# Kernel tuning notes

Hardware: AMD Instinct MI355X
Metric: run time of the kernel (lower is better)

The kernel has to match this reference:

```python
import jax, jax.numpy as jnp
import numpy as np
from jax import lax

N, CIN, H, W = 16, 3, 512, 512
BH = BW = 16  # block size (h, w); bstride == bsize so blocks tile the image
EPS = 1e-5


def setup_inputs() -> dict:
    key = jax.random.key(0)
    ks = jax.random.split(key, 32)
    def nrm(k, shape, s=0.05):
        return jax.random.normal(k, shape, jnp.float32) * s
    def bnp(k, ch):
        # rows: gamma, beta, running_mean, running_var (var kept > 0)
        u = jax.random.uniform(k, (4, ch), jnp.float32)
        return u.at[3].add(0.1)
    feat = (H // 4) * (W // 4) * 8
    return {
        "x": jax.random.normal(ks[0], (N, CIN, H, W), jnp.float32),
        "mask": jax.random.uniform(ks[1], (N, 1, H, W), jnp.float32),
        "s1_cw": nrm(ks[2], (16, CIN, 1, 1)), "s1_cb": nrm(ks[3], (16,)), "s1_bn0": bnp(ks[4], 16),
        "s1_d1w": nrm(ks[5], (32, 16, 1, 1)), "s1_d1b": nrm(ks[6], (32,)), "s1_bn1": bnp(ks[7], 32),
        "s1_d2w": nrm(ks[8], (32, 32, 3, 3)), "s1_d2b": nrm(ks[9], (32,)), "s1_bn2": bnp(ks[10], 32),
        "s1_d3w": nrm(ks[11], (16, 32, 1, 1)), "s1_d3b": nrm(ks[12], (16,)), "s1_bn3": bnp(ks[13], 16),
        "s2_cw": nrm(ks[14], (8, 16, 1, 1)), "s2_cb": nrm(ks[15], (8,)), "s2_bn0": bnp(ks[16], 8),
        "s2_d1w": nrm(ks[17], (16, 8, 1, 1)), "s2_d1b": nrm(ks[18], (16,)), "s2_bn1": bnp(ks[19], 16),
        "s2_d2w": nrm(ks[20], (16, 16, 3, 3)), "s2_d2b": nrm(ks[21], (16,)), "s2_bn2": bnp(ks[22], 16),
        "s2_d3w": nrm(ks[23], (8, 16, 1, 1)), "s2_d3b": nrm(ks[24], (8,)), "s2_bn3": bnp(ks[25], 8),
        "fc_w": nrm(ks[26], (10, feat), 0.01), "fc_b": nrm(ks[27], (10,)),
    }


def conv(x, w, b, p):
    y = lax.conv_general_dilated(x, w, (1, 1), [(p, p), (p, p)],
                                 dimension_numbers=("NCHW", "OIHW", "NCHW"))
    return y + b[None, :, None, None]


def bnorm(x, p):
    g, bt, m, v = p[0], p[1], p[2], p[3]
    scale = g * lax.rsqrt(v + EPS)
    return scale[None, :, None, None] * (x - m[None, :, None, None]) + bt[None, :, None, None]


def to_blocks(x):
    # [N,C,H,W] -> [N*nby*nbx, C, BH, BW]
    n, c, hh, ww = x.shape
    nby, nbx = hh // BH, ww // BW
    b = x.reshape(n, c, nby, BH, nbx, BW).transpose(0, 2, 4, 1, 3, 5)
    return b.reshape(n * nby * nbx, c, BH, BW), (n, nby, nbx)


def from_blocks(b, meta, c):
    n, nby, nbx = meta
    x = b.reshape(n, nby, nbx, c, BH, BW).transpose(0, 3, 1, 4, 2, 5)
    return x.reshape(n, c, nby * BH, nbx * BW)


def maxpool2(x):
    return lax.reduce_window(x, -jnp.inf, lax.max, (1, 1, 2, 2), (1, 1, 2, 2), "VALID")


def sparse_conv_block(x, mask, cw, cb, bn0, d1w, d1b, bn1, d2w, d2b, bn2, d3w, d3b, bn3):
    # reduce_mask: block is active if its mean mask value exceeds threshold
    mblocks, _ = to_blocks(mask)
    active = mblocks.mean(axis=(1, 2, 3)) > 0.5  # [N*nblocks]
    # channel path (applies to every pixel)
    xc = bnorm(jax.nn.relu(conv(x, cw, cb, 0)), bn0)
    # gather -> dense bottleneck convs per block (3x3 padded within each block) -> scatter
    blocks, meta = to_blocks(xc)
    g = bnorm(jax.nn.relu(conv(blocks, d1w, d1b, 0)), bn1)
    g = bnorm(jax.nn.relu(conv(g, d2w, d2b, 1)), bn2)
    g = bnorm(jax.nn.relu(conv(g, d3w, d3b, 0)), bn3)
    out = jnp.where(active[:, None, None, None], g, blocks)
    return from_blocks(out, meta, xc.shape[1])


def reference(x, mask, s1_cw, s1_cb, s1_bn0, s1_d1w, s1_d1b, s1_bn1, s1_d2w, s1_d2b, s1_bn2,
              s1_d3w, s1_d3b, s1_bn3, s2_cw, s2_cb, s2_bn0, s2_d1w, s2_d1b, s2_bn1,
              s2_d2w, s2_d2b, s2_bn2, s2_d3w, s2_d3b, s2_bn3, fc_w, fc_b):
    x1 = sparse_conv_block(x, mask, s1_cw, s1_cb, s1_bn0, s1_d1w, s1_d1b, s1_bn1,
                           s1_d2w, s1_d2b, s1_bn2, s1_d3w, s1_d3b, s1_bn3)
    x1 = maxpool2(x1)
    mask2 = maxpool2(mask)
    x2 = sparse_conv_block(x1, mask2, s2_cw, s2_cb, s2_bn0, s2_d1w, s2_d1b, s2_bn1,
                           s2_d2w, s2_d2b, s2_bn2, s2_d3w, s2_d3b, s2_bn3)
    x2 = maxpool2(x2)
    flat = x2.reshape(x2.shape[0], -1)  # [N, (H/4)*(W/4)*8]
    logits = flat @ fc_w.T + fc_b
    return jax.nn.softmax(logits, axis=-1)
```

## Files before the change

### kernel.cpp

```cpp
#include <hip/hip_runtime.h>
#include <math.h>


typedef __attribute__((ext_vector_type(8))) short bf16x8;
typedef __attribute__((ext_vector_type(4))) float f32x4;
typedef __attribute__((ext_vector_type(16))) float f32x16;

#define X1P_OFF 0
#define X2_OFF  16777216
#define LG_OFF  18874368
#define MS_OFF  18874624
#define P_OFF   18878720

enum : int {
  WT_S1C  = 0,
  WT_S2C  = 48,
  SC_S1BN0 = 176,
  SC_S1BN1 = 208,
  SC_S1BN2 = 272,
  SC_S1BN3 = 336,
  SC_S2BN0 = 368,
  SC_S2BN1 = 384,
  SC_S2BN2 = 416,
  SC_S2BN3 = 448,
  PH_F     = 464
};
enum : int {
  H_S1D2 = 0,
  H_S1D3 = 9216,
  H_S2D2 = 9728,
  H_S2D3 = 12288,
  H_S1D1 = 12544,
  H_S2D1 = 13568,
  PH_END = 14080
};

__device__ __forceinline__ float relu_f(float v) { return v > 0.f ? v : 0.f; }

__device__ __forceinline__ unsigned short f2bf(float f) {
  unsigned int u = __float_as_uint(f);
  unsigned int r = (u + 0x7fffu + ((u >> 16) & 1u)) >> 16;
  return (unsigned short)r;
}

__device__ __forceinline__ unsigned int pk2(float lo, float hi) {
  unsigned int r;
  asm("v_cvt_pk_bf16_f32 %0, %1, %2" : "=v"(r) : "v"(lo), "v"(hi));
  return r;
}

__device__ __forceinline__ void prep_bn(const float* __restrict__ p, int C,
                                        float* __restrict__ dst, int gid) {
  for (int i = gid; i < C; i += 8192) {
    float g = p[i], b = p[C + i], m = p[2 * C + i], v = p[3 * C + i];
    float s = g / sqrtf(v + 1e-5f);
    dst[i] = s;
    dst[C + i] = b - s * m;
  }
}

__global__ __launch_bounds__(256) void prep_kernel(
    const float* __restrict__ s1_cw, const float* __restrict__ s1_d1w,
    const float* __restrict__ s1_d2w, const float* __restrict__ s1_d3w,
    const float* __restrict__ s2_cw, const float* __restrict__ s2_d1w,
    const float* __restrict__ s2_d2w, const float* __restrict__ s2_d3w,
    const float* __restrict__ s1_bn0, const float* __restrict__ s1_bn1,
    const float* __restrict__ s1_bn2, const float* __restrict__ s1_bn3,
    const float* __restrict__ s2_bn0, const float* __restrict__ s2_bn1,
    const float* __restrict__ s2_bn2, const float* __restrict__ s2_bn3,
    float* __restrict__ P, float* __restrict__ lg, float* __restrict__ ms) {
  const int gid = blockIdx.x * 256 + threadIdx.x;
  unsigned short* PH = (unsigned short*)(P + PH_F);
  for (int i = gid; i < 48;  i += 8192) { int co = i / 3,  ci = i % 3;  P[WT_S1C + ci * 16 + co] = s1_cw[i]; }
  for (int i = gid; i < 128; i += 8192) { int co = i / 16, ci = i % 16; P[WT_S2C + ci * 8  + co] = s2_cw[i]; }
  for (int i = gid; i < 9216; i += 8192) {
    int tap = i >> 10, o = (i >> 5) & 31, ci = i & 31;
    PH[H_S1D2 + i] = f2bf(s1_d2w[o * 288 + ci * 9 + tap]);
  }
  for (int i = gid; i < 512; i += 8192) PH[H_S1D3 + i] = f2bf(s1_d3w[i]);
  for (int i = gid; i < 2560; i += 8192) {
    int p = i >> 9, o = (i >> 5) & 15, k = i & 31;
    int tp = 2 * p + (k >> 4);
    PH[H_S2D2 + i] = (tp < 9) ? f2bf(s2_d2w[o * 144 + (k & 15) * 9 + tp]) : 0;
  }
  for (int i = gid; i < 256; i += 8192) {
    int nn = i >> 4, k = i & 15;
    PH[H_S2D3 + i] = (nn < 8) ? f2bf(s2_d3w[nn * 16 + k]) : 0;
  }
  for (int i = gid; i < 1024; i += 8192) {
    int o = i >> 5, k = i & 31;
    PH[H_S1D1 + i] = (k < 16) ? f2bf(s1_d1w[o * 16 + k]) : 0;
  }
  for (int i = gid; i < 512; i += 8192) {
    int o = i >> 5, k = i & 31;
    PH[H_S2D1 + i] = (k < 8) ? f2bf(s2_d1w[o * 8 + k]) : 0;
  }
  prep_bn(s1_bn0, 16, P + SC_S1BN0, gid);
  prep_bn(s1_bn1, 32, P + SC_S1BN1, gid);
  prep_bn(s1_bn2, 32, P + SC_S1BN2, gid);
  prep_bn(s1_bn3, 16, P + SC_S1BN3, gid);
  prep_bn(s2_bn0, 8,  P + SC_S2BN0, gid);
  prep_bn(s2_bn1, 16, P + SC_S2BN1, gid);
  prep_bn(s2_bn2, 16, P + SC_S2BN2, gid);
  prep_bn(s2_bn3, 8,  P + SC_S2BN3, gid);
  if (gid < 160) lg[gid] = 0.f;
  for (int i = gid; i < 4096; i += 8192) ms[i] = 0.f;
}

__global__ __launch_bounds__(256, 4) void stage1_kernel(
    const float* __restrict__ x, const float* __restrict__ mask,
    const float* __restrict__ cbv, const float* __restrict__ d1b,
    const float* __restrict__ d2b, const float* __restrict__ d3b,
    const float* __restrict__ P, float* __restrict__ x1p,
    float* __restrict__ msum) {
  __shared__ __align__(16) unsigned char ldsb[25920];
  __shared__ float red_s[4], red_v[4];

  const int t = threadIdx.x;
  const int ty = t >> 4, tx = t & 15;
  const int b = blockIdx.x;
  const int n = b >> 10;
  const int by = (b >> 5) & 31, bx = b & 31;
  const int gy = by * 16 + ty, gx = bx * 16 + tx;

  {
    const float m = mask[(size_t)(n * 512 + gy) * 512 + gx];
    float v = fmaxf(m, __shfl_xor(m, 1, 64));
    v = fmaxf(v, __shfl_xor(v, 16, 64));
    float s = m;
    #pragma unroll
    for (int off = 32; off > 0; off >>= 1) {
      s += __shfl_down(s, off, 64);
      v += __shfl_down(v, off, 64);
    }
    if ((t & 63) == 0) { red_s[t >> 6] = s; red_v[t >> 6] = v; }
  }
  __syncthreads();

  float xin[3];
  #pragma unroll
  for (int c = 0; c < 3; ++c)
    xin[c] = x[(size_t)((n * 3 + c) * 512 + gy) * 512 + gx];

  const float* wc = P + WT_S1C;
  const float* sc0 = P + SC_S1BN0;
  float xc[16];
  {
    float a[16];
    #pragma unroll
    for (int o = 0; o < 16; ++o) a[o] = cbv[o];
    #pragma unroll
    for (int c = 0; c < 3; ++c) {
      const float v = xin[c];
      #pragma unroll
      for (int o = 0; o < 16; ++o) a[o] = fmaf(wc[c * 16 + o], v, a[o]);
    }
    #pragma unroll
    for (int o = 0; o < 16; ++o) xc[o] = fmaf(sc0[o], relu_f(a[o]), sc0[16 + o]);
  }

  const bool active = (red_s[0] + red_s[1] + red_s[2] + red_s[3]) > 128.0f;
  if (t == 0)
    atomicAdd(&msum[n * 256 + (by >> 1) * 16 + (bx >> 1)],
              (red_v[0] + red_v[1] + red_v[2] + red_v[3]) * 0.25f);

  float* const poolf = (float*)(ldsb + 20480);

  if (active) {
    const int w = t >> 6, lane = t & 63;
    const int lr = lane & 15, cb = lane >> 4;
    const unsigned short* PH = (const unsigned short*)(P + PH_F);

    if (t < 68) {
      int row, col;
      if (t < 18)      { row = 0;      col = t;      }
      else if (t < 36) { row = 17;     col = t - 18; }
      else if (t < 52) { row = t - 35; col = 0;      }
      else             { row = t - 51; col = 17;     }
      uint4* z = (uint4*)(ldsb + (row * 18 + col) * 80);
      const uint4 z4 = make_uint4(0u, 0u, 0u, 0u);
      z[0] = z4; z[1] = z4; z[2] = z4; z[3] = z4;
    }
    {
      unsigned int pk[8];
      #pragma unroll
      for (int i = 0; i < 8; ++i) pk[i] = pk2(xc[2 * i], xc[2 * i + 1]);
      uint4* dst = (uint4*)(ldsb + ((ty + 1) * 18 + (tx + 1)) * 80);
      dst[0] = make_uint4(pk[0], pk[1], pk[2], pk[3]);
      dst[1] = make_uint4(pk[4], pk[5], pk[6], pk[7]);
    }

    {
      bf16x8 w1f[2];
      #pragma unroll
      for (int ct = 0; ct < 2; ++ct)
        w1f[ct] = *(const bf16x8*)(PH + H_S1D1 + (ct * 16 + lr) * 32 + cb * 8);
      f32x4 acc1[2][4];
      #pragma unroll
      for (int ct = 0; ct < 2; ++ct) {
        const float4 bb = *(const float4*)(d1b + ct * 16 + cb * 4);
        #pragma unroll
        for (int nt = 0; nt < 4; ++nt) {
          acc1[ct][nt][0] = bb.x; acc1[ct][nt][1] = bb.y;
          acc1[ct][nt][2] = bb.z; acc1[ct][nt][3] = bb.w;
        }
      }
      #pragma unroll
      for (int nt = 0; nt < 4; ++nt) {
        bf16x8 xcf;
        if (cb < 2) xcf = *(const bf16x8*)(ldsb + ((w * 4 + nt + 1) * 18 + lr + 1) * 80 + cb * 16);
        else        xcf = (bf16x8)(short)0;
        #pragma unroll
        for (int ct = 0; ct < 2; ++ct)
          acc1[ct][nt] = __builtin_amdgcn_mfma_f32_16x16x32_bf16(w1f[ct], xcf, acc1[ct][nt], 0, 0, 0);
      }
      #pragma unroll
      for (int ct = 0; ct < 2; ++ct) {
        const float4 s1s = *(const float4*)(P + SC_S1BN1 + ct * 16 + cb * 4);
        const float4 s1h = *(const float4*)(P + SC_S1BN1 + 32 + ct * 16 + cb * 4);
        #pragma unroll
        for (int nt = 0; nt < 4; ++nt) {
          const unsigned base = ((w * 4 + nt + 1) * 18 + lr + 1) * 80 + (ct * 16 + cb * 4) * 2;
          uint2 wv;
          wv.x = pk2(fmaf(s1s.x, relu_f(acc1[ct][nt][0]), s1h.x),
                     fmaf(s1s.y, relu_f(acc1[ct][nt][1]), s1h.y));
          wv.y = pk2(fmaf(s1s.z, relu_f(acc1[ct][nt][2]), s1h.z),
                     fmaf(s1s.w, relu_f(acc1[ct][nt][3]), s1h.w));
          *(uint2*)(ldsb + base) = wv;
        }
      }
    }
    __syncthreads();

    const int lane31 = lane & 31;
    const int prow = lane31 >> 4, pcol = lane & 15, kh = lane >> 5;
    f32x16 acc2[2];
    {
      float4 bb2[4];
      #pragma unroll
      for (int g = 0; g < 4; ++g) bb2[g] = *(const float4*)(d2b + 8 * g + 4 * kh);
      #pragma unroll
      for (int mti = 0; mti < 2; ++mti) {
        #pragma unroll
        for (int g = 0; g < 4; ++g) {
          acc2[mti][4 * g + 0] = bb2[g].x; acc2[mti][4 * g + 1] = bb2[g].y;
          acc2[mti][4 * g + 2] = bb2[g].z; acc2[mti][4 * g + 3] = bb2[g].w;
        }
      }
    }
    #pragma clang loop unroll(disable)
    for (int dy = 0; dy < 3; ++dy) {
      bf16x8 aw[3][2];
      #pragma unroll
      for (int dx = 0; dx < 3; ++dx)
        #pragma unroll
        for (int ch = 0; ch < 2; ++ch)
          aw[dx][ch] = *(const bf16x8*)(PH + H_S1D2 + ((dy * 3 + dx) * 32 + lane31) * 32 + ch * 16 + kh * 8);
      const unsigned char* bp = ldsb + ((w * 4 + prow + dy) * 18 + pcol) * 80 + kh * 16;
      #pragma unroll
      for (int dx = 0; dx < 3; ++dx)
        #pragma unroll
        for (int mti = 0; mti < 2; ++mti)
          #pragma unroll
          for (int ch = 0; ch < 2; ++ch) {
            const bf16x8 bf = *(const bf16x8*)(bp + mti * 2880 + dx * 80 + ch * 32);
            acc2[mti] = __builtin_amdgcn_mfma_f32_32x32x16_bf16(aw[dx][ch], bf, acc2[mti], 0, 0, 0);
          }
    }
    __syncthreads();

    #pragma unroll
    for (int mti = 0; mti < 2; ++mti) {
      const int pix = (w * 2 + mti) * 32 + lane31;
      #pragma unroll
      for (int g = 0; g < 4; ++g) {
        const float4 ss = *(const float4*)(P + SC_S1BN2 + 8 * g + 4 * kh);
        const float4 sh = *(const float4*)(P + SC_S1BN2 + 32 + 8 * g + 4 * kh);
        uint2 wv;
        wv.x = pk2(fmaf(ss.x, relu_f(acc2[mti][4 * g + 0]), sh.x),
                   fmaf(ss.y, relu_f(acc2[mti][4 * g + 1]), sh.y));
        wv.y = pk2(fmaf(ss.z, relu_f(acc2[mti][4 * g + 2]), sh.z),
                   fmaf(ss.w, relu_f(acc2[mti][4 * g + 3]), sh.w));
        *(uint2*)(ldsb + pix * 80 + (8 * g + 4 * kh) * 2) = wv;
      }
    }
    __syncthreads();

    const bf16x8 b3 = *(const bf16x8*)(PH + H_S1D3 + lr * 32 + cb * 8);
    const float bias3v = d3b[lr];
    const float sc3v = P[SC_S1BN3 + lr], sh3v = P[SC_S1BN3 + 16 + lr];
    f32x4 acc3[4];
    #pragma unroll
    for (int mt = 0; mt < 4; ++mt) {
      acc3[mt][0] = bias3v; acc3[mt][1] = bias3v; acc3[mt][2] = bias3v; acc3[mt][3] = bias3v;
      const bf16x8 a3 = *(const bf16x8*)(ldsb + (w * 64 + mt * 16 + lr) * 80 + cb * 16);
      acc3[mt] = __builtin_amdgcn_mfma_f32_16x16x32_bf16(a3, b3, acc3[mt], 0, 0, 0);
    }
    #pragma unroll
    for (int mtp = 0; mtp < 2; ++mtp) {
      float o0[4], o1[4];
      #pragma unroll
      for (int r = 0; r < 4; ++r) {
        o0[r] = fmaf(sc3v, relu_f(acc3[2 * mtp][r]), sh3v);
        o1[r] = fmaf(sc3v, relu_f(acc3[2 * mtp + 1][r]), sh3v);
      }
      #pragma unroll
      for (int rp = 0; rp < 2; ++rp) {
        const float m = fmaxf(fmaxf(o0[2 * rp], o0[2 * rp + 1]),
                              fmaxf(o1[2 * rp], o1[2 * rp + 1]));
        poolf[lr * 68 + (w * 2 + mtp) * 8 + cb * 2 + rp] = m;
      }
    }
  } else {
    float* ldsf = (float*)ldsb;
    {
      float* pw = &ldsf[t * 20];
      #pragma unroll
      for (int c = 0; c < 16; ++c) pw[c] = xc[c];
    }
    __syncthreads();
    {
      const int pp = t & 63, cg = t >> 6;
      const int py = pp >> 3, px = pp & 7;
      const float* r0 = &ldsf[((2 * py) * 16 + 2 * px) * 20 + cg * 4];
      const float* r2 = &ldsf[((2 * py + 1) * 16 + 2 * px) * 20 + cg * 4];
      const float4 v0 = *(const float4*)(r0);
      const float4 v1 = *(const float4*)(r0 + 20);
      const float4 v2 = *(const float4*)(r2);
      const float4 v3 = *(const float4*)(r2 + 20);
      poolf[(cg * 4 + 0) * 68 + py * 8 + px] = fmaxf(fmaxf(v0.x, v1.x), fmaxf(v2.x, v3.x));
      poolf[(cg * 4 + 1) * 68 + py * 8 + px] = fmaxf(fmaxf(v0.y, v1.y), fmaxf(v2.y, v3.y));
      poolf[(cg * 4 + 2) * 68 + py * 8 + px] = fmaxf(fmaxf(v0.z, v1.z), fmaxf(v2.z, v3.z));
      poolf[(cg * 4 + 3) * 68 + py * 8 + px] = fmaxf(fmaxf(v0.w, v1.w), fmaxf(v2.w, v3.w));
    }
  }

  __syncthreads();
  {
    const int ch = t >> 4, idx = t & 15, yy = idx >> 1, h = idx & 1;
    const uint4 v = *(const uint4*)(poolf + ch * 68 + yy * 8 + h * 4);
    const size_t ob = ((((size_t)n * 16 + (by >> 1)) * 16 + (bx >> 1)) * 16 + ch) * 256
                      + (size_t)((by & 1) * 8 + yy) * 16 + (bx & 1) * 8 + h * 4;
    *(uint4*)(x1p + ob) = v;
  }
}

__global__ __launch_bounds__(256, 5) void stage2_kernel(
    const float* __restrict__ msum,
    const float* __restrict__ cbv, const float* __restrict__ d1b,
    const float* __restrict__ d2b, const float* __restrict__ d3b,
    const float* __restrict__ P, const float* __restrict__ x1p,
    float* __restrict__ x2) {
  __shared__ __align__(16) unsigned char ldsb2[15552];

  const int t = threadIdx.x;
  const int ty = t >> 4, tx = t & 15;
  const int b = blockIdx.x;
  const int n = b >> 8;
  const int BY = (b >> 4) & 15, BX = b & 15;

  const bool active = msum[b] > 128.0f;

  const float* xb = x1p + (size_t)b * 4096 + ty * 16 + tx;
  float xin[16];
  #pragma unroll
  for (int c = 0; c < 16; ++c) xin[c] = xb[c * 256];

  const float* wc = P + WT_S2C;
  const float* sc0 = P + SC_S2BN0;
  float xc[8];
  {
    float a[8];
    #pragma unroll
    for (int o = 0; o < 8; ++o) a[o] = cbv[o];
    #pragma unroll
    for (int c = 0; c < 16; ++c) {
      const float v = xin[c];
      #pragma unroll
      for (int o = 0; o < 8; ++o) a[o] = fmaf(wc[c * 8 + o], v, a[o]);
    }
    #pragma unroll
    for (int o = 0; o < 8; ++o) xc[o] = fmaf(sc0[o], relu_f(a[o]), sc0[8 + o]);
  }

  float* const poolf = (float*)(ldsb2 + 12288);

  if (active) {
    const int w = t >> 6, lane = t & 63;
    const int lr = lane & 15, cb = lane >> 4;
    const unsigned short* PH = (const unsigned short*)(P + PH_F);

    if (t < 68) {
      int row, col;
      if (t < 18)      { row = 0;      col = t;      }
      else if (t < 36) { row = 17;     col = t - 18; }
      else if (t < 52) { row = t - 35; col = 0;      }
      else             { row = t - 51; col = 17;     }
      uint4* z = (uint4*)(ldsb2 + (row * 18 + col) * 48);
      const uint4 z4 = make_uint4(0u, 0u, 0u, 0u);
      z[0] = z4; z[1] = z4;
    }
    {
      unsigned int pk[4];
      #pragma unroll
      for (int i = 0; i < 4; ++i) pk[i] = pk2(xc[2 * i], xc[2 * i + 1]);
      *(uint4*)(ldsb2 + ((ty + 1) * 18 + (tx + 1)) * 48) = make_uint4(pk[0], pk[1], pk[2], pk[3]);
    }

    {
      const bf16x8 w1f = *(const bf16x8*)(PH + H_S2D1 + lr * 32 + cb * 8);
      f32x4 acc1[4];
      {
        const float4 bb = *(const float4*)(d1b + cb * 4);
        #pragma unroll
        for (int nt = 0; nt < 4; ++nt) {
          acc1[nt][0] = bb.x; acc1[nt][1] = bb.y; acc1[nt][2] = bb.z; acc1[nt][3] = bb.w;
        }
      }
      #pragma unroll
      for (int nt = 0; nt < 4; ++nt) {
        bf16x8 xcf;
        if (cb == 0) xcf = *(const bf16x8*)(ldsb2 + ((w * 4 + nt + 1) * 18 + lr + 1) * 48);
        else         xcf = (bf16x8)(short)0;
        acc1[nt] = __builtin_amdgcn_mfma_f32_16x16x32_bf16(w1f, xcf, acc1[nt], 0, 0, 0);
      }
      {
        const float4 s1s = *(const float4*)(P + SC_S2BN1 + cb * 4);
        const float4 s1h = *(const float4*)(P + SC_S2BN1 + 16 + cb * 4);
        #pragma unroll
        for (int nt = 0; nt < 4; ++nt) {
          const unsigned base = ((w * 4 + nt + 1) * 18 + lr + 1) * 48 + cb * 8;
          uint2 wv;
          wv.x = pk2(fmaf(s1s.x, relu_f(acc1[nt][0]), s1h.x),
                     fmaf(s1s.y, relu_f(acc1[nt][1]), s1h.y));
          wv.y = pk2(fmaf(s1s.z, relu_f(acc1[nt][2]), s1h.z),
                     fmaf(s1s.w, relu_f(acc1[nt][3]), s1h.w));
          *(uint2*)(ldsb2 + base) = wv;
        }
      }
    }
    __syncthreads();

    f32x4 acc2[4];
    {
      const float4 bb = *(const float4*)(d2b + cb * 4);
      #pragma unroll
      for (int nt = 0; nt < 4; ++nt) {
        acc2[nt][0] = bb.x; acc2[nt][1] = bb.y; acc2[nt][2] = bb.z; acc2[nt][3] = bb.w;
      }
    }
    #pragma clang loop unroll(disable)
    for (int p = 0; p < 5; ++p) {
      const bf16x8 bwp = *(const bf16x8*)(PH + H_S2D2 + (p * 16 + lr) * 32 + cb * 8);
      const int tp = (p < 4) ? (2 * p + (cb >> 1)) : 8;
      const int dy = (tp >= 6) ? 2 : ((tp >= 3) ? 1 : 0);
      const int dx = tp - dy * 3;
      #pragma unroll
      for (int nt = 0; nt < 4; ++nt) {
        const bf16x8 af = *(const bf16x8*)(ldsb2 + ((w * 4 + nt + dy) * 18 + lr + dx) * 48 + (cb & 1) * 16);
        acc2[nt] = __builtin_amdgcn_mfma_f32_16x16x32_bf16(bwp, af, acc2[nt], 0, 0, 0);
      }
    }
    __syncthreads();

    {
      const float4 s2s = *(const float4*)(P + SC_S2BN2 + cb * 4);
      const float4 s2h = *(const float4*)(P + SC_S2BN2 + 16 + cb * 4);
      #pragma unroll
      for (int nt = 0; nt < 4; ++nt) {
        const int pix = w * 64 + nt * 16 + lr;
        const unsigned base = pix * 48 + cb * 8;
        uint2 wv;
        wv.x = pk2(fmaf(s2s.x, relu_f(acc2[nt][0]), s2h.x),
                   fmaf(s2s.y, relu_f(acc2[nt][1]), s2h.y));
        wv.y = pk2(fmaf(s2s.z, relu_f(acc2[nt][2]), s2h.z),
                   fmaf(s2s.w, relu_f(acc2[nt][3]), s2h.w));
        *(uint2*)(ldsb2 + base) = wv;
      }
    }
    __syncthreads();

    bf16x8 b3;
    if (cb < 2) b3 = *(const bf16x8*)(PH + H_S2D3 + lr * 16 + cb * 8);
    else        b3 = (bf16x8)(short)0;
    const float bias3v = (lr < 8) ? d3b[lr] : 0.f;
    const float sc3v = (lr < 8) ? P[SC_S2BN3 + lr] : 0.f;
    const float sh3v = (lr < 8) ? P[SC_S2BN3 + 8 + lr] : 0.f;
    f32x4 acc3[4];
    #pragma unroll
    for (int mt = 0; mt < 4; ++mt) {
      acc3[mt][0] = bias3v; acc3[mt][1] = bias3v; acc3[mt][2] = bias3v; acc3[mt][3] = bias3v;
      bf16x8 a3;
      if (cb < 2) a3 = *(const bf16x8*)(ldsb2 + (w * 64 + mt * 16 + lr) * 48 + cb * 16);
      else        a3 = (bf16x8)(short)0;
      acc3[mt] = __builtin_amdgcn_mfma_f32_16x16x32_bf16(a3, b3, acc3[mt], 0, 0, 0);
    }
    if (lr < 8) {
      #pragma unroll
      for (int mtp = 0; mtp < 2; ++mtp) {
        float o0[4], o1[4];
        #pragma unroll
        for (int r = 0; r < 4; ++r) {
          o0[r] = fmaf(sc3v, relu_f(acc3[2 * mtp][r]), sh3v);
          o1[r] = fmaf(sc3v, relu_f(acc3[2 * mtp + 1][r]), sh3v);
        }
        #pragma unroll
        for (int rp = 0; rp < 2; ++rp) {
          const float m = fmaxf(fmaxf(o0[2 * rp], o0[2 * rp + 1]),
                                fmaxf(o1[2 * rp], o1[2 * rp + 1]));
          poolf[lr * 68 + (w * 2 + mtp) * 8 + cb * 2 + rp] = m;
        }
      }
    }
  } else {
    float* ldsf = (float*)ldsb2;
    {
      float* pw = &ldsf[t * 12];
      #pragma unroll
      for (int c = 0; c < 8; ++c) pw[c] = xc[c];
    }
    __syncthreads();
    if (t < 128) {
      const int pp = t & 63, cg = t >> 6;
      const int py = pp >> 3, px = pp & 7;
      const float* r0 = &ldsf[((2 * py) * 16 + 2 * px) * 12 + cg * 4];
      const float* r2 = &ldsf[((2 * py + 1) * 16 + 2 * px) * 12 + cg * 4];
      const float4 v0 = *(const float4*)(r0);
      const float4 v1 = *(const float4*)(r0 + 12);
      const float4 v2 = *(const float4*)(r2);
      const float4 v3 = *(const float4*)(r2 + 12);
      poolf[(cg * 4 + 0) * 68 + py * 8 + px] = fmaxf(fmaxf(v0.x, v1.x), fmaxf(v2.x, v3.x));
      poolf[(cg * 4 + 1) * 68 + py * 8 + px] = fmaxf(fmaxf(v0.y, v1.y), fmaxf(v2.y, v3.y));
      poolf[(cg * 4 + 2) * 68 + py * 8 + px] = fmaxf(fmaxf(v0.z, v1.z), fmaxf(v2.z, v3.z));
      poolf[(cg * 4 + 3) * 68 + py * 8 + px] = fmaxf(fmaxf(v0.w, v1.w), fmaxf(v2.w, v3.w));
    }
  }

  __syncthreads();
  if (t < 128) {
    const int ch = t >> 4, idx = t & 15, yy = idx >> 1, h = idx & 1;
    const uint4 v = *(const uint4*)(poolf + ch * 68 + yy * 8 + h * 4);
    const size_t ob = ((size_t)(n * 8 + ch) * 128 + (BY * 8 + yy)) * 128 + BX * 8 + h * 4;
    *(uint4*)(x2 + ob) = v;
  }
}

__global__ __launch_bounds__(256) void fc_kernel(const float* __restrict__ x2,
                                                 const float* __restrict__ fcw,
                                                 const float* __restrict__ fcb,
                                                 float* __restrict__ logits) {
  __shared__ float red[4];
  const int wg = blockIdx.x, t = threadIdx.x;
  const int sp = wg & 7, k = (wg >> 3) % 10, n = wg / 80;
  const float4* xa = (const float4*)(x2 + (size_t)n * 131072) + sp * 4096;
  const float4* wa = (const float4*)(fcw + (size_t)k * 131072) + sp * 4096;
  float s = 0.f;
  #pragma unroll 4
  for (int i = t; i < 4096; i += 256) {
    const float4 a = xa[i], b = wa[i];
    s = fmaf(a.x, b.x, fmaf(a.y, b.y, fmaf(a.z, b.z, fmaf(a.w, b.w, s))));
  }
  #pragma unroll
  for (int off = 32; off > 0; off >>= 1) s += __shfl_down(s, off, 64);
  if ((t & 63) == 0) red[t >> 6] = s;
  __syncthreads();
  if (t == 0) {
    float tot = red[0] + red[1] + red[2] + red[3];
    if (sp == 0) tot += fcb[k];
    atomicAdd(&logits[n * 10 + k], tot);
  }
}

__global__ void softmax_kernel(const float* __restrict__ logits, float* __restrict__ out) {
  const int t = threadIdx.x;
  if (t < 16) {
    float l[10], mx = -1e30f;
    #pragma unroll
    for (int k = 0; k < 10; ++k) { l[k] = logits[t * 10 + k]; mx = fmaxf(mx, l[k]); }
    float sum = 0.f;
    #pragma unroll
    for (int k = 0; k < 10; ++k) { l[k] = expf(l[k] - mx); sum += l[k]; }
    const float inv = 1.f / sum;
    #pragma unroll
    for (int k = 0; k < 10; ++k) out[t * 10 + k] = l[k] * inv;
  }
}

extern "C" void kernel_launch(void* const* d_in, const int* in_sizes, int n_in,
                              void* d_out, int out_size, void* d_ws, size_t ws_size,
                              hipStream_t stream) {
  const float* x      = (const float*)d_in[0];
  const float* mask   = (const float*)d_in[1];
  const float* s1_cw  = (const float*)d_in[2];
  const float* s1_cb  = (const float*)d_in[3];
  const float* s1_bn0 = (const float*)d_in[4];
  const float* s1_d1w = (const float*)d_in[5];
  const float* s1_d1b = (const float*)d_in[6];
  const float* s1_bn1 = (const float*)d_in[7];
  const float* s1_d2w = (const float*)d_in[8];
  const float* s1_d2b = (const float*)d_in[9];
  const float* s1_bn2 = (const float*)d_in[10];
  const float* s1_d3w = (const float*)d_in[11];
  const float* s1_d3b = (const float*)d_in[12];
  const float* s1_bn3 = (const float*)d_in[13];
  const float* s2_cw  = (const float*)d_in[14];
  const float* s2_cb  = (const float*)d_in[15];
  const float* s2_bn0 = (const float*)d_in[16];
  const float* s2_d1w = (const float*)d_in[17];
  const float* s2_d1b = (const float*)d_in[18];
  const float* s2_bn1 = (const float*)d_in[19];
  const float* s2_d2w = (const float*)d_in[20];
  const float* s2_d2b = (const float*)d_in[21];
  const float* s2_bn2 = (const float*)d_in[22];
  const float* s2_d3w = (const float*)d_in[23];
  const float* s2_d3b = (const float*)d_in[24];
  const float* s2_bn3 = (const float*)d_in[25];
  const float* fc_w   = (const float*)d_in[26];
  const float* fc_b   = (const float*)d_in[27];

  float* ws  = (float*)d_ws;
  float* x1p = ws + X1P_OFF;
  float* x2  = ws + X2_OFF;
  float* lg  = ws + LG_OFF;
  float* ms  = ws + MS_OFF;
  float* P   = ws + P_OFF;

  prep_kernel<<<32, 256, 0, stream>>>(s1_cw, s1_d1w, s1_d2w, s1_d3w,
                                      s2_cw, s2_d1w, s2_d2w, s2_d3w,
                                      s1_bn0, s1_bn1, s1_bn2, s1_bn3,
                                      s2_bn0, s2_bn1, s2_bn2, s2_bn3, P, lg, ms);
  stage1_kernel<<<16 * 32 * 32, 256, 0, stream>>>(x, mask, s1_cb, s1_d1b, s1_d2b, s1_d3b, P, x1p, ms);
  stage2_kernel<<<16 * 16 * 16, 256, 0, stream>>>(ms, s2_cb, s2_d1b, s2_d2b, s2_d3b, P, x1p, x2);
  fc_kernel<<<1280, 256, 0, stream>>>(x2, fc_w, fc_b, lg);
  softmax_kernel<<<1, 64, 0, stream>>>(lg, (float*)d_out);
}
```

Baseline: 276.4 us.

## Store pooled stage-1 output as bf16 and use 32x32 MFMA for 1x1 convs

The pooled intermediate between stage 1 and stage 2 is now written and read as bf16 instead of fp32, which halves that tensor's global memory traffic and shrinks the workspace. The first 1x1 bottleneck conv in both stages switches from 16x16x32 MFMA tiles with zero-padded K to 32x32x16 MFMA tiles, with the weight packing in the prep kernel changed to match. This cuts wasted MFMA work on padding, but adds bf16 rounding on an activation that was previously kept in fp32.

```diff
diff --git a/kernel.cpp b/kernel.cpp
--- a/kernel.cpp
+++ b/kernel.cpp
@@ -6,11 +6,11 @@
 typedef __attribute__((ext_vector_type(4))) float f32x4;
 typedef __attribute__((ext_vector_type(16))) float f32x16;
 
-#define X1P_OFF 0
-#define X2_OFF  16777216
-#define LG_OFF  18874368
-#define MS_OFF  18874624
-#define P_OFF   18878720
+#define X1P_USH_OFF 0
+#define X2_OFF  8388608
+#define LG_OFF  10485760
+#define MS_OFF  10486016
+#define P_OFF   10490112
 
 enum : int {
   WT_S1C  = 0,
@@ -49,6 +49,10 @@
   return r;
 }
 
+__device__ __forceinline__ float bf2f(unsigned short u) {
+  return __uint_as_float((unsigned int)u << 16);
+}
+
 __device__ __forceinline__ void prep_bn(const float* __restrict__ p, int C,
                                         float* __restrict__ dst, int gid) {
   for (int i = gid; i < C; i += 8192) {
@@ -87,13 +91,10 @@
     int nn = i >> 4, k = i & 15;
     PH[H_S2D3 + i] = (nn < 8) ? f2bf(s2_d3w[nn * 16 + k]) : 0;
   }
-  for (int i = gid; i < 1024; i += 8192) {
-    int o = i >> 5, k = i & 31;
-    PH[H_S1D1 + i] = (k < 16) ? f2bf(s1_d1w[o * 16 + k]) : 0;
-  }
+  for (int i = gid; i < 512; i += 8192) PH[H_S1D1 + i] = f2bf(s1_d1w[i]);
   for (int i = gid; i < 512; i += 8192) {
-    int o = i >> 5, k = i & 31;
-    PH[H_S2D1 + i] = (k < 8) ? f2bf(s2_d1w[o * 8 + k]) : 0;
+    int co = i >> 4, k = i & 15;
+    PH[H_S2D1 + i] = (co < 16 && k < 8) ? f2bf(s2_d1w[co * 8 + k]) : 0;
   }
   prep_bn(s1_bn0, 16, P + SC_S1BN0, gid);
   prep_bn(s1_bn1, 32, P + SC_S1BN1, gid);
@@ -111,7 +112,7 @@
     const float* __restrict__ x, const float* __restrict__ mask,
     const float* __restrict__ cbv, const float* __restrict__ d1b,
     const float* __restrict__ d2b, const float* __restrict__ d3b,
-    const float* __restrict__ P, float* __restrict__ x1p,
+    const float* __restrict__ P, unsigned short* __restrict__ x1p,
     float* __restrict__ msum) {
   __shared__ __align__(16) unsigned char ldsb[25920];
   __shared__ float red_s[4], red_v[4];
@@ -169,6 +170,7 @@
   if (active) {
     const int w = t >> 6, lane = t & 63;
     const int lr = lane & 15, cb = lane >> 4;
+    const int lane31 = lane & 31, kh = lane >> 5;
     const unsigned short* PH = (const unsigned short*)(P + PH_F);
 
     if (t < 68) {
@@ -191,49 +193,42 @@
     }
 
     {
-      bf16x8 w1f[2];
-      #pragma unroll
-      for (int ct = 0; ct < 2; ++ct)
-        w1f[ct] = *(const bf16x8*)(PH + H_S1D1 + (ct * 16 + lr) * 32 + cb * 8);
-      f32x4 acc1[2][4];
-      #pragma unroll
-      for (int ct = 0; ct < 2; ++ct) {
-        const float4 bb = *(const float4*)(d1b + ct * 16 + cb * 4);
-        #pragma unroll
-        for (int nt = 0; nt < 4; ++nt) {
-          acc1[ct][nt][0] = bb.x; acc1[ct][nt][1] = bb.y;
-          acc1[ct][nt][2] = bb.z; acc1[ct][nt][3] = bb.w;
-        }
-      }
-      #pragma unroll
-      for (int nt = 0; nt < 4; ++nt) {
-        bf16x8 xcf;
-        if (cb < 2) xcf = *(const bf16x8*)(ldsb + ((w * 4 + nt + 1) * 18 + lr + 1) * 80 + cb * 16);
-        else        xcf = (bf16x8)(short)0;
-        #pragma unroll
-        for (int ct = 0; ct < 2; ++ct)
-          acc1[ct][nt] = __builtin_amdgcn_mfma_f32_16x16x32_bf16(w1f[ct], xcf, acc1[ct][nt], 0, 0, 0);
-      }
-      #pragma unroll
-      for (int ct = 0; ct < 2; ++ct) {
-        const float4 s1s = *(const float4*)(P + SC_S1BN1 + ct * 16 + cb * 4);
-        const float4 s1h = *(const float4*)(P + SC_S1BN1 + 32 + ct * 16 + cb * 4);
-        #pragma unroll
-        for (int nt = 0; nt < 4; ++nt) {
-          const unsigned base = ((w * 4 + nt + 1) * 18 + lr + 1) * 80 + (ct * 16 + cb * 4) * 2;
+      const bf16x8 w1f = *(const bf16x8*)(PH + H_S1D1 + lane31 * 16 + kh * 8);
+      f32x16 acc1[2];
+      #pragma unroll
+      for (int nt = 0; nt < 2; ++nt)
+        #pragma unroll
+        for (int g = 0; g < 4; ++g) {
+          const float4 bb = *(const float4*)(d1b + 8 * g + 4 * kh);
+          acc1[nt][4 * g + 0] = bb.x; acc1[nt][4 * g + 1] = bb.y;
+          acc1[nt][4 * g + 2] = bb.z; acc1[nt][4 * g + 3] = bb.w;
+        }
+      #pragma unroll
+      for (int nt = 0; nt < 2; ++nt) {
+        const int p = w * 64 + nt * 32 + lane31;
+        const bf16x8 xcf = *(const bf16x8*)(ldsb + (((p >> 4) + 1) * 18 + (p & 15) + 1) * 80 + kh * 16);
+        acc1[nt] = __builtin_amdgcn_mfma_f32_32x32x16_bf16(w1f, xcf, acc1[nt], 0, 0, 0);
+      }
+      #pragma unroll
+      for (int nt = 0; nt < 2; ++nt) {
+        const int p = w * 64 + nt * 32 + lane31;
+        const unsigned pbase = (((p >> 4) + 1) * 18 + (p & 15) + 1) * 80;
+        #pragma unroll
+        for (int g = 0; g < 4; ++g) {
+          const float4 ss = *(const float4*)(P + SC_S1BN1 + 8 * g + 4 * kh);
+          const float4 sh = *(const float4*)(P + SC_S1BN1 + 32 + 8 * g + 4 * kh);
           uint2 wv;
-          wv.x = pk2(fmaf(s1s.x, relu_f(acc1[ct][nt][0]), s1h.x),
-                     fmaf(s1s.y, relu_f(acc1[ct][nt][1]), s1h.y));
-          wv.y = pk2(fmaf(s1s.z, relu_f(acc1[ct][nt][2]), s1h.z),
-                     fmaf(s1s.w, relu_f(acc1[ct][nt][3]), s1h.w));
-          *(uint2*)(ldsb + base) = wv;
-        }
-      }
-    }
-    __syncthreads();
-
-    const int lane31 = lane & 31;
-    const int prow = lane31 >> 4, pcol = lane & 15, kh = lane >> 5;
+          wv.x = pk2(fmaf(ss.x, relu_f(acc1[nt][4 * g + 0]), sh.x),
+                     fmaf(ss.y, relu_f(acc1[nt][4 * g + 1]), sh.y));
+          wv.y = pk2(fmaf(ss.z, relu_f(acc1[nt][4 * g + 2]), sh.z),
+                     fmaf(ss.w, relu_f(acc1[nt][4 * g + 3]), sh.w));
+          *(uint2*)(ldsb + pbase + (8 * g + 4 * kh) * 2) = wv;
+        }
+      }
+    }
+    __syncthreads();
+
+    const int prow = lane31 >> 4, pcol = lane & 15;
     f32x16 acc2[2];
     {
       float4 bb2[4];
@@ -336,12 +331,16 @@
   }
 
   __syncthreads();
-  {
-    const int ch = t >> 4, idx = t & 15, yy = idx >> 1, h = idx & 1;
-    const uint4 v = *(const uint4*)(poolf + ch * 68 + yy * 8 + h * 4);
-    const size_t ob = ((((size_t)n * 16 + (by >> 1)) * 16 + (bx >> 1)) * 16 + ch) * 256
-                      + (size_t)((by & 1) * 8 + yy) * 16 + (bx & 1) * 8 + h * 4;
-    *(uint4*)(x1p + ob) = v;
+  if (t < 128) {
+    const int ch = t >> 3, yy = t & 7;
+    const float* pr = poolf + ch * 68 + yy * 8;
+    uint4 v;
+    v.x = pk2(pr[0], pr[1]); v.y = pk2(pr[2], pr[3]);
+    v.z = pk2(pr[4], pr[5]); v.w = pk2(pr[6], pr[7]);
+    unsigned short* dst = x1p
+        + ((((size_t)n * 16 + (by >> 1)) * 16 + (bx >> 1)) * 16 + ch) * 256
+        + (size_t)((by & 1) * 8 + yy) * 16 + (bx & 1) * 8;
+    *(uint4*)dst = v;
   }
 }
 
@@ -349,7 +348,7 @@
     const float* __restrict__ msum,
     const float* __restrict__ cbv, const float* __restrict__ d1b,
     const float* __restrict__ d2b, const float* __restrict__ d3b,
-    const float* __restrict__ P, const float* __restrict__ x1p,
+    const float* __restrict__ P, const unsigned short* __restrict__ x1p,
     float* __restrict__ x2) {
   __shared__ __align__(16) unsigned char ldsb2[15552];
 
@@ -361,10 +360,10 @@
 
   const bool active = msum[b] > 128.0f;
 
-  const float* xb = x1p + (size_t)b * 4096 + ty * 16 + tx;
+  const unsigned short* xb = x1p + (size_t)b * 4096 + ty * 16 + tx;
   float xin[16];
   #pragma unroll
-  for (int c = 0; c < 16; ++c) xin[c] = xb[c * 256];
+  for (int c = 0; c < 16; ++c) xin[c] = bf2f(xb[c * 256]);
 
   const float* wc = P + WT_S2C;
   const float* sc0 = P + SC_S2BN0;
@@ -388,6 +387,7 @@
   if (active) {
     const int w = t >> 6, lane = t & 63;
     const int lr = lane & 15, cb = lane >> 4;
+    const int lane31 = lane & 31, kh = lane >> 5;
     const unsigned short* PH = (const unsigned short*)(P + PH_F);
 
     if (t < 68) {
@@ -408,34 +408,46 @@
     }
 
     {
-      const bf16x8 w1f = *(const bf16x8*)(PH + H_S2D1 + lr * 32 + cb * 8);
-      f32x4 acc1[4];
-      {
-        const float4 bb = *(const float4*)(d1b + cb * 4);
-        #pragma unroll
-        for (int nt = 0; nt < 4; ++nt) {
-          acc1[nt][0] = bb.x; acc1[nt][1] = bb.y; acc1[nt][2] = bb.z; acc1[nt][3] = bb.w;
-        }
-      }
-      #pragma unroll
-      for (int nt = 0; nt < 4; ++nt) {
+      const bf16x8 w1f = *(const bf16x8*)(PH + H_S2D1 + lane31 * 16 + kh * 8);
+      f32x16 acc1[2];
+      #pragma unroll
+      for (int nt = 0; nt < 2; ++nt)
+        #pragma unroll
+        for (int g = 0; g < 2; ++g) {
+          const float4 bb = *(const float4*)(d1b + 8 * g + 4 * kh);
+          acc1[nt][4 * g + 0] = bb.x; acc1[nt][4 * g + 1] = bb.y;
+          acc1[nt][4 * g + 2] = bb.z; acc1[nt][4 * g + 3] = bb.w;
+        }
+      #pragma unroll
+      for (int nt = 0; nt < 2; ++nt) {
+        #pragma unroll
+        for (int g = 2; g < 4; ++g) {
+          acc1[nt][4 * g + 0] = 0.f; acc1[nt][4 * g + 1] = 0.f;
+          acc1[nt][4 * g + 2] = 0.f; acc1[nt][4 * g + 3] = 0.f;
+        }
+      }
+      #pragma unroll
+      for (int nt = 0; nt < 2; ++nt) {
+        const int p = w * 64 + nt * 32 + lane31;
         bf16x8 xcf;
-        if (cb == 0) xcf = *(const bf16x8*)(ldsb2 + ((w * 4 + nt + 1) * 18 + lr + 1) * 48);
+        if (kh == 0) xcf = *(const bf16x8*)(ldsb2 + (((p >> 4) + 1) * 18 + (p & 15) + 1) * 48);
         else         xcf = (bf16x8)(short)0;
-        acc1[nt] = __builtin_amdgcn_mfma_f32_16x16x32_bf16(w1f, xcf, acc1[nt], 0, 0, 0);
-      }
-      {
-        const float4 s1s = *(const float4*)(P + SC_S2BN1 + cb * 4);
-        const float4 s1h = *(const float4*)(P + SC_S2BN1 + 16 + cb * 4);
-        #pragma unroll
-        for (int nt = 0; nt < 4; ++nt) {
-          const unsigned base = ((w * 4 + nt + 1) * 18 + lr + 1) * 48 + cb * 8;
+        acc1[nt] = __builtin_amdgcn_mfma_f32_32x32x16_bf16(w1f, xcf, acc1[nt], 0, 0, 0);
+      }
+      #pragma unroll
+      for (int nt = 0; nt < 2; ++nt) {
+        const int p = w * 64 + nt * 32 + lane31;
+        const unsigned pbase = (((p >> 4) + 1) * 18 + (p & 15) + 1) * 48;
+        #pragma unroll
+        for (int g = 0; g < 2; ++g) {
+          const float4 ss = *(const float4*)(P + SC_S2BN1 + 8 * g + 4 * kh);
+          const float4 sh = *(const float4*)(P + SC_S2BN1 + 16 + 8 * g + 4 * kh);
           uint2 wv;
-          wv.x = pk2(fmaf(s1s.x, relu_f(acc1[nt][0]), s1h.x),
-                     fmaf(s1s.y, relu_f(acc1[nt][1]), s1h.y));
-          wv.y = pk2(fmaf(s1s.z, relu_f(acc1[nt][2]), s1h.z),
-                     fmaf(s1s.w, relu_f(acc1[nt][3]), s1h.w));
-          *(uint2*)(ldsb2 + base) = wv;
+          wv.x = pk2(fmaf(ss.x, relu_f(acc1[nt][4 * g + 0]), sh.x),
+                     fmaf(ss.y, relu_f(acc1[nt][4 * g + 1]), sh.y));
+          wv.y = pk2(fmaf(ss.z, relu_f(acc1[nt][4 * g + 2]), sh.z),
+                     fmaf(ss.w, relu_f(acc1[nt][4 * g + 3]), sh.w));
+          *(uint2*)(ldsb2 + pbase + (8 * g + 4 * kh) * 2) = wv;
         }
       }
     }
@@ -619,7 +631,7 @@
   const float* fc_b   = (const float*)d_in[27];
 
   float* ws  = (float*)d_ws;
-  float* x1p = ws + X1P_OFF;
+  unsigned short* x1p = (unsigned short*)d_ws;
   float* x2  = ws + X2_OFF;
   float* lg  = ws + LG_OFF;
   float* ms  = ws + MS_OFF;
```

Result: faster. 270.7 us (-2.1%).
